# Optimization experiments

Hardware: AMD Instinct MI355X
Metric: run time of the kernel (lower is better)

The kernel has to match this reference:

```python
import jax, jax.numpy as jnp
import numpy as np

B, L, C = 128, 512, 321
PRED = 336
S = 4
K = 25  # moving_avg kernel
EPS = 1e-5
N = L // S          # 128
H = 2048 // S       # 512


def setup_inputs() -> dict:
    key = jax.random.key(0)
    ks = jax.random.split(key, 16)
    def w(k, shape, fan_in):
        return jax.random.uniform(k, shape, jnp.float32, -1.0, 1.0) / np.sqrt(fan_in)
    return {
        "x": jax.random.normal(ks[0], (B, L, C), jnp.float32),
        "revin_w": jnp.ones((C,), jnp.float32),
        "revin_b": jnp.zeros((C,), jnp.float32),
        "W11": w(ks[1], (N, H), N), "b11": w(ks[2], (H,), N),
        "W12": w(ks[3], (H, N), H), "b12": w(ks[4], (N,), H),
        "W21": w(ks[5], (N, H), N), "b21": w(ks[6], (H,), N),
        "W22": w(ks[7], (H, N), H), "b22": w(ks[8], (N,), H),
        "W_tr": w(ks[9], (L, PRED), L), "b_tr": w(ks[10], (PRED,), L),
        "W_se": w(ks[11], (L, PRED), L), "b_se": w(ks[12], (PRED,), L),
    }


def reference(x, revin_w, revin_b, W11, b11, W12, b12, W21, b21, W22, b22,
              W_tr, b_tr, W_se, b_se):
    # RevIN norm (statistics are detached in the original)
    mean = jax.lax.stop_gradient(jnp.mean(x, axis=1, keepdims=True))
    std = jax.lax.stop_gradient(
        jnp.sqrt(jnp.var(x, axis=1, keepdims=True) + EPS))
    xn = (x - mean) / std * revin_w + revin_b  # [B, L, C]

    # Decomp: replicate-pad along time then moving average of width K
    front = jnp.repeat(xn[:, 0:1, :], K - 1 - (K - 1) // 2, axis=1)
    end = jnp.repeat(xn[:, -1:, :], (K - 1) // 2, axis=1)
    padded = jnp.concatenate([front, xn, end], axis=1)  # [B, L+K-1, C]
    cs = jnp.concatenate(
        [jnp.zeros((B, 1, C), padded.dtype), jnp.cumsum(padded, axis=1)], axis=1)
    trend = (cs[:, K:, :] - cs[:, :-K, :]) / K  # [B, L, C]
    seasonal = xn - trend

    trend_p = jnp.transpose(trend, (0, 2, 1))      # [B, C, L]
    seasonal_p = jnp.transpose(seasonal, (0, 2, 1))  # [B, C, L]

    # Trend head: Linear L -> PRED
    trend_out = jnp.einsum('bcl,lp->bcp', trend_p, W_tr) + b_tr

    # Seasonal head: Splitting (strided interleave) = reshape + transpose
    xs = seasonal_p.reshape(B, C, N, S).transpose(0, 1, 3, 2)  # [B, C, S, N]
    h = jnp.matmul(jax.nn.gelu(jnp.matmul(xs, W11) + b11, approximate=False), W12) + b12
    h = jnp.matmul(jax.nn.gelu(jnp.matmul(h, W21) + b21, approximate=False), W22) + b22
    # Catting is the exact inverse interleave
    sea = h.transpose(0, 1, 3, 2).reshape(B, C, L)  # [B, C, L]
    sea_out = jnp.einsum('bcl,lp->bcp', sea, W_se) + b_se

    out = jnp.transpose(trend_out + sea_out, (0, 2, 1))  # [B, PRED, C]

    # RevIN denorm
    out = (out - revin_b) / (revin_w + EPS * EPS)
    out = out * std + mean
    return out
```

## Files before the change

### kernel.cpp

```cpp
#include <hip/hip_runtime.h>
#include <math.h>

#define BB   128
#define LL   512
#define CC   321
#define PREDD 336

using bf16x8  = __attribute__((ext_vector_type(8))) __bf16;
using floatx4 = __attribute__((ext_vector_type(4))) float;
using uintx4  = __attribute__((ext_vector_type(4))) unsigned int;
typedef unsigned short u16;
typedef unsigned int u32;

#define MFMA16(a,b,c) __builtin_amdgcn_mfma_f32_16x16x32_bf16(a,b,c,0,0,0)

__device__ __forceinline__ u16 f2bf(float f){
    union { float f; unsigned u; } v; v.f = f;
    unsigned r = v.u + 0x7FFFu + ((v.u >> 16) & 1u);
    return (u16)(r >> 16);
}

__device__ __forceinline__ float fgelu(float x){
    float u = x*(0.7978845608f + 0.035677408f*x*x);
    float a = fminf(u*2.8853900818f, 80.f);
    float t = __builtin_amdgcn_exp2f(a);
    return x*t*__builtin_amdgcn_rcpf(1.f + t);
}

__device__ __forceinline__ int swz128(int r, int s){ return r*128 + (((s & 8) | ((s ^ r) & 7)) << 3); }
__device__ __forceinline__ int swz64 (int r, int s){ return r*64  + (((s ^ r) & 7) << 3); }

__device__ __forceinline__ void dma16(const u16* g, const u16* l){
    __builtin_amdgcn_global_load_lds(
        (const __attribute__((address_space(1))) u32*)g,
        (__attribute__((address_space(3))) u32*)l, 16, 0, 0);
}

__global__ void prep_k(const float* __restrict__ W11, const float* __restrict__ W12,
                       const float* __restrict__ W21, const float* __restrict__ W22,
                       const float* __restrict__ Wtr, const float* __restrict__ Wse,
                       u16* __restrict__ BT1, u16* __restrict__ BT2,
                       u16* __restrict__ BT3, u16* __restrict__ BT4,
                       u16* __restrict__ BT5)
{
    int idx = blockIdx.x * 256 + threadIdx.x;
    if (idx < 65536){
        int h = idx >> 7, k = idx & 127;
        BT1[idx] = f2bf(W11[k*512 + h]);
        BT3[idx] = f2bf(W21[k*512 + h]);
        int n = idx >> 9, k2 = idx & 511;
        BT2[idx] = f2bf(W12[k2*128 + n]);
        BT4[idx] = f2bf(W22[k2*128 + n]);
    }
    if (idx < 393216){
        int p = idx >> 10, k = idx & 1023;
        float v = 0.f;
        if (p < PREDD){
            if (k < 512) v = Wtr[k*PREDD + p];
            else { int kk = k - 512; int s = kk >> 7; int n = kk & 127; v = Wse[(4*n + s)*PREDD + p]; }
        }
        BT5[idx] = f2bf(v);
    }
}

#define XT(t,c) xt[((t)<<4) + (((t)>>5)<<1) + (c)]
__global__ __launch_bounds__(256) void decomp_k(
    const float* __restrict__ x, const float* __restrict__ rw, const float* __restrict__ rb,
    u16* __restrict__ Afin, u16* __restrict__ xs, float2* __restrict__ stats)
{
    __shared__ float xt[8240];
    __shared__ float red[2][16][16];
    __shared__ float sh_m[16], sh_istd[16];
    int b = blockIdx.x / 21, ct = blockIdx.x % 21;
    int tid = threadIdx.x;

    int cl = tid & 15, lp = tid >> 4;
    int c = ct*16 + cl;
    bool valid = c < CC;
    const float* xb = x + (size_t)b*LL*CC;
    float s = 0.f, q = 0.f;
    for (int i = 0; i < 32; ++i){
        int t = lp + 16*i;
        float v = valid ? xb[(size_t)t*CC + c] : 0.f;
        XT(t, cl) = v;
        s += v; q += v*v;
    }
    red[0][lp][cl] = s; red[1][lp][cl] = q;
    __syncthreads();
    if (tid < 16){
        float ss = 0.f, qq = 0.f;
        for (int j = 0; j < 16; ++j){ ss += red[0][j][tid]; qq += red[1][j][tid]; }
        float m  = ss * (1.f/512.f);
        float var = qq * (1.f/512.f) - m*m;
        float sd = sqrtf(var + 1e-5f);
        sh_m[tid] = m; sh_istd[tid] = 1.f/sd;
        int cc = ct*16 + tid;
        if (cc < CC) stats[(size_t)b*CC + cc] = make_float2(m, sd);
    }
    __syncthreads();

    int ch = tid >> 4, tp = tid & 15;
    int c2 = ct*16 + ch;
    if (c2 >= CC) return;
    float m = sh_m[ch], istd = sh_istd[ch];
    float w = rw[c2] * istd, bbv = rb[c2];
    size_t bc = (size_t)b*CC + c2;
    u16* tr  = Afin + bc*1024;
    u16* xsr = xs   + bc*512;
    int t0 = tp*32;

    float win = 0.f;
#pragma unroll
    for (int d = -12; d <= 12; ++d){
        int u = t0 + d; u = u < 0 ? 0 : (u > 511 ? 511 : u);
        win += XT(u, ch);
    }
    u16 trbuf[8];
    u16 xsbuf[4][8];
#pragma unroll
    for (int i = 0; i < 32; ++i){
        int t = t0 + i;
        float Ax = win * (1.f/25.f);
        float xv = XT(t, ch);
        trbuf[i & 7] = f2bf((Ax - m)*w + bbv);
        xsbuf[i & 3][i >> 2] = f2bf((xv - Ax)*w);
        if ((i & 7) == 7)
            *(uintx4*)(tr + t0 + (i & ~7)) = *(const uintx4*)trbuf;
        int uo = t - 12; uo = uo < 0 ? 0 : uo;
        int un = t + 13; un = un > 511 ? 511 : un;
        win += XT(un, ch) - XT(uo, ch);
    }
#pragma unroll
    for (int s4 = 0; s4 < 4; ++s4)
        *(uintx4*)(xsr + s4*128 + tp*8) = *(const uintx4*)xsbuf[s4];
}

#define RW1 0
#define RH  8192
#define RW2 16384
__global__ __launch_bounds__(256, 2) void mlp_fused_k(
    const u16* __restrict__ xs,
    const u16* __restrict__ BT1, const float* __restrict__ b11,
    const u16* __restrict__ BT2, const float* __restrict__ b12,
    const u16* __restrict__ BT3, const float* __restrict__ b21,
    const u16* __restrict__ BT4, const float* __restrict__ b22,
    u16* __restrict__ Afin)
{
    __shared__ u16 lds[32768];
    const int tid = threadIdx.x;
    const int row0 = blockIdx.x * 128;
    const int lane = tid & 63;
    const int wv = tid >> 6;
    const int wm = wv & 1, wn = wv >> 1;
    const int quad = lane >> 4, cl = lane & 15;

#pragma unroll
    for (int i = 0; i < 8; ++i){
        int qq = (wv*8 + i)*64 + lane;
        int r = qq >> 4, sp = qq & 15;
        int s = (sp & 8) | ((sp ^ r) & 7);
        dma16(xs + (size_t)(row0 + r)*128 + s*8, lds + RW2 + qq*8);
    }
    __syncthreads();

    bf16x8 afrag[4][4];
#pragma unroll
    for (int mt = 0; mt < 4; ++mt)
#pragma unroll
        for (int ks = 0; ks < 4; ++ks)
            afrag[mt][ks] = *(const bf16x8*)(lds + RW2 + swz128(wm*64 + mt*16 + cl, ks*4 + quad));
    __syncthreads();

#pragma unroll
    for (int i = 0; i < 4; ++i){
        int qq = (wv*4 + i)*64 + lane;
        { int r = qq >> 4, sp = qq & 15; int s = (sp & 8) | ((sp ^ r) & 7);
          dma16(BT1 + (size_t)r*128 + s*8, lds + RW1 + qq*8); }
        { int r = qq >> 3, p = qq & 7; int s = (p ^ r) & 7;
          dma16(BT2 + (size_t)r*512 + s*8, lds + RW2 + qq*8); }
    }
    __syncthreads();

    for (int mlp = 0; mlp < 2; ++mlp){
        const float* ba = mlp ? b21 : b11;
        const float* bb = mlp ? b22 : b12;

        floatx4 Yacc[16];
#pragma unroll
        for (int i = 0; i < 16; ++i) Yacc[i] = (floatx4){0.f,0.f,0.f,0.f};

        for (int hc = 0; hc < 8; ++hc){
            const int g = mlp*8 + hc;
            floatx4 hacc[8];
#pragma unroll
            for (int i = 0; i < 8; ++i) hacc[i] = (floatx4){0.f,0.f,0.f,0.f};
#pragma unroll
            for (int ks = 0; ks < 4; ++ks){
                bf16x8 b0 = *(const bf16x8*)(lds + RW1 + swz128(wn*32 + cl,      ks*4 + quad));
                bf16x8 b1 = *(const bf16x8*)(lds + RW1 + swz128(wn*32 + 16 + cl, ks*4 + quad));
#pragma unroll
                for (int mt = 0; mt < 4; ++mt){
                    hacc[mt*2+0] = MFMA16(afrag[mt][ks], b0, hacc[mt*2+0]);
                    hacc[mt*2+1] = MFMA16(afrag[mt][ks], b1, hacc[mt*2+1]);
                }
            }
            {
                int h0 = wn*32 + cl, h1v = h0 + 16;
                float bav0 = ba[hc*64 + h0];
                float bav1 = ba[hc*64 + h1v];
#pragma unroll
                for (int mt = 0; mt < 4; ++mt){
                    floatx4 v0 = hacc[mt*2], v1 = hacc[mt*2+1];
#pragma unroll
                    for (int i = 0; i < 4; ++i){
                        int r = wm*64 + mt*16 + quad*4 + i;
                        lds[RH + r*64 + (((h0 >> 3) ^ r) & 7)*8 + (h0 & 7)]   = f2bf(fgelu(v0[i] + bav0));
                        lds[RH + r*64 + (((h1v >> 3) ^ r) & 7)*8 + (h1v & 7)] = f2bf(fgelu(v1[i] + bav1));
                    }
                }
            }
            __syncthreads();
            if (g < 15){
                const u16* w1s = ((g+1) & 8) ? BT3 : BT1;
                const u16* w2s = ((g+1) & 8) ? BT4 : BT2;
                const int hb = ((g+1) & 7) * 64;
                const int slot = RW2 + ((hc+1) & 1) * 8192;
#pragma unroll
                for (int i = 0; i < 4; ++i){
                    int qq = (wv*4 + i)*64 + lane;
                    if (hc < 7){
                        int r = qq >> 4, sp = qq & 15; int s = (sp & 8) | ((sp ^ r) & 7);
                        dma16(w1s + (size_t)(hb + r)*128 + s*8, lds + RW1 + qq*8);
                    }
                    int r2 = qq >> 3, p2 = qq & 7; int s2 = (p2 ^ r2) & 7;
                    dma16(w2s + (size_t)r2*512 + hb + s2*8, lds + slot + qq*8);
                }
            }
            {
                const int W2p = RW2 + (hc & 1) * 8192;
#pragma unroll
                for (int ks = 0; ks < 2; ++ks){
                    bf16x8 a2[4], b2[4];
#pragma unroll
                    for (int mt = 0; mt < 4; ++mt) a2[mt] = *(const bf16x8*)(lds + RH  + swz64(wm*64 + mt*16 + cl, ks*4 + quad));
#pragma unroll
                    for (int nt = 0; nt < 4; ++nt) b2[nt] = *(const bf16x8*)(lds + W2p + swz64(wn*64 + nt*16 + cl, ks*4 + quad));
#pragma unroll
                    for (int mt = 0; mt < 4; ++mt)
#pragma unroll
                        for (int nt = 0; nt < 4; ++nt)
                            Yacc[mt*4+nt] = MFMA16(a2[mt], b2[nt], Yacc[mt*4+nt]);
                }
            }
            __syncthreads();
        }

        if (mlp == 0){
#pragma unroll
            for (int mt = 0; mt < 4; ++mt)
#pragma unroll
                for (int nt = 0; nt < 4; ++nt){
                    int c = wn*64 + nt*16 + cl;
                    float bv = bb[c];
                    floatx4 v = Yacc[mt*4+nt];
#pragma unroll
                    for (int i = 0; i < 4; ++i){
                        int r = wm*64 + mt*16 + quad*4 + i;
                        lds[swz128(r, c >> 3) + (c & 7)] = f2bf(v[i] + bv);
                    }
                }
            __syncthreads();
#pragma unroll
            for (int mt = 0; mt < 4; ++mt)
#pragma unroll
                for (int ks = 0; ks < 4; ++ks)
                    afrag[mt][ks] = *(const bf16x8*)(lds + swz128(wm*64 + mt*16 + cl, ks*4 + quad));
            __syncthreads();
#pragma unroll
            for (int i = 0; i < 4; ++i){
                int qq = (wv*4 + i)*64 + lane;
                int r = qq >> 4, sp = qq & 15; int s = (sp & 8) | ((sp ^ r) & 7);
                dma16(BT3 + (size_t)r*128 + s*8, lds + RW1 + qq*8);
            }
            __syncthreads();
        } else {
#pragma unroll
            for (int mt = 0; mt < 4; ++mt)
#pragma unroll
                for (int nt = 0; nt < 4; ++nt){
                    int c = wn*64 + nt*16 + cl;
                    float bv = bb[c];
                    floatx4 v = Yacc[mt*4+nt];
#pragma unroll
                    for (int i = 0; i < 4; ++i){
                        int gr = row0 + wm*64 + mt*16 + quad*4 + i;
                        Afin[(size_t)(gr>>2)*1024 + 512 + (size_t)(gr&3)*128 + c] = f2bf(v[i] + bv);
                    }
                }
        }
    }
}

__global__ __launch_bounds__(256, 2) void head_gemm_k(
    const u16* __restrict__ A, const u16* __restrict__ BT,
    float* __restrict__ Cf,
    const float* __restrict__ bias, const float* __restrict__ bias2,
    const float* __restrict__ rw, const float* __restrict__ rb,
    const float2* __restrict__ stats)
{
    __shared__ u16 lds[32768];
    const int id = blockIdx.x;
    const int xcd = id & 7, slot = id >> 3;
    const int g8 = slot / 3, j = slot - g8*3;
    const int by = xcd + 8*g8;
    if (by >= 321) return;
    const int row0 = by * 128, col0 = j * 128;

    const int tid = threadIdx.x;
    const int lane = tid & 63;
    const int wv = tid >> 6;
    const int wm = wv & 1, wn = wv >> 1;
    const int quad = lane >> 4, cl = lane & 15;

    const int qbase = wv*4*64 + lane;

#pragma unroll
    for (int i = 0; i < 4; ++i){
        int qq = qbase + i*64;
        int r = qq >> 3, p = qq & 7; int s = (p ^ r) & 7;
        dma16(A  + (size_t)(row0 + r)*1024 + s*8, lds + qq*8);
        dma16(BT + (size_t)(col0 + r)*1024 + s*8, lds + 16384 + qq*8);
    }
    __syncthreads();

    floatx4 acc[16];
#pragma unroll
    for (int i = 0; i < 16; ++i) acc[i] = (floatx4){0.f,0.f,0.f,0.f};

    for (int it = 0; it < 16; ++it){
        const int cur = (it & 1) * 8192;
        if (it < 15){
            const int nxt = ((it+1) & 1) * 8192;
            const int k0 = (it+1) * 64;
#pragma unroll
            for (int i = 0; i < 4; ++i){
                int qq = qbase + i*64;
                int r = qq >> 3, p = qq & 7; int s = (p ^ r) & 7;
                dma16(A  + (size_t)(row0 + r)*1024 + k0 + s*8, lds + nxt + qq*8);
                dma16(BT + (size_t)(col0 + r)*1024 + k0 + s*8, lds + 16384 + nxt + qq*8);
            }
        }
#pragma unroll
        for (int kk = 0; kk < 2; ++kk){
            bf16x8 af[4], bfr[4];
#pragma unroll
            for (int mt = 0; mt < 4; ++mt) af[mt]  = *(const bf16x8*)(lds + cur + swz64(wm*64 + mt*16 + cl, kk*4 + quad));
#pragma unroll
            for (int nt = 0; nt < 4; ++nt) bfr[nt] = *(const bf16x8*)(lds + 16384 + cur + swz64(wn*64 + nt*16 + cl, kk*4 + quad));
#pragma unroll
            for (int mt = 0; mt < 4; ++mt)
#pragma unroll
                for (int nt = 0; nt < 4; ++nt)
                    acc[mt*4+nt] = MFMA16(af[mt], bfr[nt], acc[mt*4+nt]);
        }
        __syncthreads();
    }

#pragma unroll
    for (int mt = 0; mt < 4; ++mt)
#pragma unroll
        for (int nt = 0; nt < 4; ++nt){
            floatx4 v = acc[mt*4+nt];
            int gc = col0 + wn*64 + nt*16 + cl;
            if (gc >= PREDD) continue;
            float bsum = bias[gc] + bias2[gc];
#pragma unroll
            for (int i = 0; i < 4; ++i){
                int gr = row0 + wm*64 + mt*16 + quad*4 + i;
                float val = v[i] + bsum;
                int bv2 = gr / CC;
                int c  = gr - bv2*CC;
                val = (val - rb[c]) / (rw[c] + 1e-10f);
                float2 st = stats[gr];
                val = val*st.y + st.x;
                Cf[(size_t)bv2*(PREDD*CC) + (size_t)gc*CC + c] = val;
            }
        }
}

extern "C" void kernel_launch(void* const* d_in, const int* in_sizes, int n_in,
                              void* d_out, int out_size, void* d_ws, size_t ws_size,
                              hipStream_t stream)
{
    const float* x   = (const float*)d_in[0];
    const float* rvw = (const float*)d_in[1];
    const float* rvb = (const float*)d_in[2];
    const float* W11 = (const float*)d_in[3];
    const float* b11 = (const float*)d_in[4];
    const float* W12 = (const float*)d_in[5];
    const float* b12 = (const float*)d_in[6];
    const float* W21 = (const float*)d_in[7];
    const float* b21 = (const float*)d_in[8];
    const float* W22 = (const float*)d_in[9];
    const float* b22 = (const float*)d_in[10];
    const float* Wtr = (const float*)d_in[11];
    const float* btr = (const float*)d_in[12];
    const float* Wse = (const float*)d_in[13];
    const float* bse = (const float*)d_in[14];
    float* out = (float*)d_out;

    char* ws = (char*)d_ws;
    u16* BT1 = (u16*)(ws + 0);
    u16* BT2 = (u16*)(ws + 131072);
    u16* BT3 = (u16*)(ws + 262144);
    u16* BT4 = (u16*)(ws + 393216);
    u16* BT5 = (u16*)(ws + 524288);
    float2* stats = (float2*)(ws + 1310720);
    u16* Afin = (u16*)(ws + 1639424);
    u16* xs   = (u16*)(ws + 85787648);

    hipLaunchKernelGGL(prep_k, dim3(1536), dim3(256), 0, stream,
                       W11, W12, W21, W22, Wtr, Wse, BT1, BT2, BT3, BT4, BT5);
    hipLaunchKernelGGL(decomp_k, dim3(128*21), dim3(256), 0, stream,
                       x, rvw, rvb, Afin, xs, stats);
    hipLaunchKernelGGL(mlp_fused_k, dim3(1284), dim3(256), 0, stream,
                       xs, BT1, b11, BT2, b12, BT3, b21, BT4, b22, Afin);
    hipLaunchKernelGGL(head_gemm_k, dim3(984), dim3(256), 0, stream,
                       Afin, BT5, out, btr, bse, rvw, rvb, stats);
}
```

Before: 514.0 us.

## Give each wave private hidden scratch and double-buffer weight chunks in fused MLP

Result: faster. 451.2 us (-12.2%).

```diff
diff --git a/kernel.cpp b/kernel.cpp
--- a/kernel.cpp
+++ b/kernel.cpp
@@ -135,9 +135,8 @@
         *(uintx4*)(xsr + s4*128 + tp*8) = *(const uintx4*)xsbuf[s4];
 }
 
-#define RW1 0
-#define RH  8192
-#define RW2 16384
+#define SL1 16384
+#define HS  32768
 __global__ __launch_bounds__(256, 2) void mlp_fused_k(
     const u16* __restrict__ xs,
     const u16* __restrict__ BT1, const float* __restrict__ b11,
@@ -146,159 +145,142 @@
     const u16* __restrict__ BT4, const float* __restrict__ b22,
     u16* __restrict__ Afin)
 {
-    __shared__ u16 lds[32768];
+    __shared__ u16 lds[40960];
     const int tid = threadIdx.x;
     const int row0 = blockIdx.x * 128;
     const int lane = tid & 63;
     const int wv = tid >> 6;
-    const int wm = wv & 1, wn = wv >> 1;
     const int quad = lane >> 4, cl = lane & 15;
-
-#pragma unroll
-    for (int i = 0; i < 8; ++i){
-        int qq = (wv*8 + i)*64 + lane;
-        int r = qq >> 4, sp = qq & 15;
-        int s = (sp & 8) | ((sp ^ r) & 7);
-        dma16(xs + (size_t)(row0 + r)*128 + s*8, lds + RW2 + qq*8);
-    }
-    __syncthreads();
-
-    bf16x8 afrag[4][4];
-#pragma unroll
-    for (int mt = 0; mt < 4; ++mt)
-#pragma unroll
-        for (int ks = 0; ks < 4; ++ks)
-            afrag[mt][ks] = *(const bf16x8*)(lds + RW2 + swz128(wm*64 + mt*16 + cl, ks*4 + quad));
-    __syncthreads();
+    const int wrow = row0 + wv*32;
+    u16* hscr = lds + HS + wv*2048;
+    const int rdswz = ((cl >> 2) & 3) << 4;
 
 #pragma unroll
     for (int i = 0; i < 4; ++i){
         int qq = (wv*4 + i)*64 + lane;
         { int r = qq >> 4, sp = qq & 15; int s = (sp & 8) | ((sp ^ r) & 7);
-          dma16(BT1 + (size_t)r*128 + s*8, lds + RW1 + qq*8); }
+          dma16(BT1 + (size_t)r*128 + s*8, lds + qq*8); }
         { int r = qq >> 3, p = qq & 7; int s = (p ^ r) & 7;
-          dma16(BT2 + (size_t)r*512 + s*8, lds + RW2 + qq*8); }
-    }
+          dma16(BT2 + (size_t)r*512 + s*8, lds + 8192 + qq*8); }
+    }
+    bf16x8 afrag[2][4];
+#pragma unroll
+    for (int mt = 0; mt < 2; ++mt)
+#pragma unroll
+        for (int ks = 0; ks < 4; ++ks)
+            afrag[mt][ks] = *(const bf16x8*)(xs + (size_t)(wrow + mt*16 + cl)*128 + ks*32 + quad*8);
+
+    floatx4 Yacc[16];
+#pragma unroll
+    for (int i = 0; i < 16; ++i) Yacc[i] = (floatx4){0.f,0.f,0.f,0.f};
+
     __syncthreads();
 
-    for (int mlp = 0; mlp < 2; ++mlp){
-        const float* ba = mlp ? b21 : b11;
-        const float* bb = mlp ? b22 : b12;
-
-        floatx4 Yacc[16];
-#pragma unroll
-        for (int i = 0; i < 16; ++i) Yacc[i] = (floatx4){0.f,0.f,0.f,0.f};
-
-        for (int hc = 0; hc < 8; ++hc){
-            const int g = mlp*8 + hc;
-            floatx4 hacc[8];
-#pragma unroll
-            for (int i = 0; i < 8; ++i) hacc[i] = (floatx4){0.f,0.f,0.f,0.f};
-#pragma unroll
-            for (int ks = 0; ks < 4; ++ks){
-                bf16x8 b0 = *(const bf16x8*)(lds + RW1 + swz128(wn*32 + cl,      ks*4 + quad));
-                bf16x8 b1 = *(const bf16x8*)(lds + RW1 + swz128(wn*32 + 16 + cl, ks*4 + quad));
-#pragma unroll
-                for (int mt = 0; mt < 4; ++mt){
-                    hacc[mt*2+0] = MFMA16(afrag[mt][ks], b0, hacc[mt*2+0]);
-                    hacc[mt*2+1] = MFMA16(afrag[mt][ks], b1, hacc[mt*2+1]);
-                }
-            }
-            {
-                int h0 = wn*32 + cl, h1v = h0 + 16;
-                float bav0 = ba[hc*64 + h0];
-                float bav1 = ba[hc*64 + h1v];
-#pragma unroll
-                for (int mt = 0; mt < 4; ++mt){
-                    floatx4 v0 = hacc[mt*2], v1 = hacc[mt*2+1];
-#pragma unroll
-                    for (int i = 0; i < 4; ++i){
-                        int r = wm*64 + mt*16 + quad*4 + i;
-                        lds[RH + r*64 + (((h0 >> 3) ^ r) & 7)*8 + (h0 & 7)]   = f2bf(fgelu(v0[i] + bav0));
-                        lds[RH + r*64 + (((h1v >> 3) ^ r) & 7)*8 + (h1v & 7)] = f2bf(fgelu(v1[i] + bav1));
-                    }
-                }
-            }
-            __syncthreads();
-            if (g < 15){
-                const u16* w1s = ((g+1) & 8) ? BT3 : BT1;
-                const u16* w2s = ((g+1) & 8) ? BT4 : BT2;
-                const int hb = ((g+1) & 7) * 64;
-                const int slot = RW2 + ((hc+1) & 1) * 8192;
-#pragma unroll
-                for (int i = 0; i < 4; ++i){
-                    int qq = (wv*4 + i)*64 + lane;
-                    if (hc < 7){
-                        int r = qq >> 4, sp = qq & 15; int s = (sp & 8) | ((sp ^ r) & 7);
-                        dma16(w1s + (size_t)(hb + r)*128 + s*8, lds + RW1 + qq*8);
-                    }
-                    int r2 = qq >> 3, p2 = qq & 7; int s2 = (p2 ^ r2) & 7;
-                    dma16(w2s + (size_t)r2*512 + hb + s2*8, lds + slot + qq*8);
-                }
-            }
-            {
-                const int W2p = RW2 + (hc & 1) * 8192;
-#pragma unroll
-                for (int ks = 0; ks < 2; ++ks){
-                    bf16x8 a2[4], b2[4];
-#pragma unroll
-                    for (int mt = 0; mt < 4; ++mt) a2[mt] = *(const bf16x8*)(lds + RH  + swz64(wm*64 + mt*16 + cl, ks*4 + quad));
-#pragma unroll
-                    for (int nt = 0; nt < 4; ++nt) b2[nt] = *(const bf16x8*)(lds + W2p + swz64(wn*64 + nt*16 + cl, ks*4 + quad));
-#pragma unroll
-                    for (int mt = 0; mt < 4; ++mt)
-#pragma unroll
-                        for (int nt = 0; nt < 4; ++nt)
-                            Yacc[mt*4+nt] = MFMA16(a2[mt], b2[nt], Yacc[mt*4+nt]);
-                }
-            }
-            __syncthreads();
-        }
-
-        if (mlp == 0){
-#pragma unroll
-            for (int mt = 0; mt < 4; ++mt)
-#pragma unroll
-                for (int nt = 0; nt < 4; ++nt){
-                    int c = wn*64 + nt*16 + cl;
-                    float bv = bb[c];
-                    floatx4 v = Yacc[mt*4+nt];
-#pragma unroll
-                    for (int i = 0; i < 4; ++i){
-                        int r = wm*64 + mt*16 + quad*4 + i;
-                        lds[swz128(r, c >> 3) + (c & 7)] = f2bf(v[i] + bv);
-                    }
-                }
-            __syncthreads();
-#pragma unroll
-            for (int mt = 0; mt < 4; ++mt)
-#pragma unroll
-                for (int ks = 0; ks < 4; ++ks)
-                    afrag[mt][ks] = *(const bf16x8*)(lds + swz128(wm*64 + mt*16 + cl, ks*4 + quad));
-            __syncthreads();
+    for (int g = 0; g < 16; ++g){
+        const int cur = (g & 1) ? SL1 : 0;
+        const int nxt = (g & 1) ? 0 : SL1;
+        if (g < 15){
+            const u16* w1s = ((g+1) & 8) ? BT3 : BT1;
+            const u16* w2s = ((g+1) & 8) ? BT4 : BT2;
+            const int hb = ((g+1) & 7) * 64;
 #pragma unroll
             for (int i = 0; i < 4; ++i){
                 int qq = (wv*4 + i)*64 + lane;
-                int r = qq >> 4, sp = qq & 15; int s = (sp & 8) | ((sp ^ r) & 7);
-                dma16(BT3 + (size_t)r*128 + s*8, lds + RW1 + qq*8);
-            }
-            __syncthreads();
-        } else {
-#pragma unroll
-            for (int mt = 0; mt < 4; ++mt)
-#pragma unroll
-                for (int nt = 0; nt < 4; ++nt){
-                    int c = wn*64 + nt*16 + cl;
-                    float bv = bb[c];
-                    floatx4 v = Yacc[mt*4+nt];
-#pragma unroll
-                    for (int i = 0; i < 4; ++i){
-                        int gr = row0 + wm*64 + mt*16 + quad*4 + i;
-                        Afin[(size_t)(gr>>2)*1024 + 512 + (size_t)(gr&3)*128 + c] = f2bf(v[i] + bv);
+                { int r = qq >> 4, sp = qq & 15; int s = (sp & 8) | ((sp ^ r) & 7);
+                  dma16(w1s + (size_t)(hb + r)*128 + s*8, lds + nxt + qq*8); }
+                { int r = qq >> 3, p = qq & 7; int s = (p ^ r) & 7;
+                  dma16(w2s + (size_t)r*512 + hb + s*8, lds + nxt + 8192 + qq*8); }
+            }
+        }
+        const float* ba = (g & 8) ? b21 : b11;
+        const int hc = g & 7;
+
+        floatx4 hacc[8];
+#pragma unroll
+        for (int i = 0; i < 8; ++i) hacc[i] = (floatx4){0.f,0.f,0.f,0.f};
+#pragma unroll
+        for (int ks = 0; ks < 4; ++ks){
+            bf16x8 bfr[4];
+#pragma unroll
+            for (int nt = 0; nt < 4; ++nt)
+                bfr[nt] = *(const bf16x8*)(lds + cur + swz128(nt*16 + cl, ks*4 + quad));
+#pragma unroll
+            for (int mt = 0; mt < 2; ++mt)
+#pragma unroll
+                for (int nt = 0; nt < 4; ++nt)
+                    hacc[mt*4+nt] = MFMA16(afrag[mt][ks], bfr[nt], hacc[mt*4+nt]);
+        }
+#pragma unroll
+        for (int mt = 0; mt < 2; ++mt)
+#pragma unroll
+            for (int nt = 0; nt < 4; ++nt){
+                floatx4 v = hacc[mt*4+nt];
+                int h = nt*16 + cl;
+                float bav = ba[hc*64 + h];
+#pragma unroll
+                for (int i = 0; i < 4; ++i){
+                    int r = mt*16 + quad*4 + i;
+                    hscr[r*64 + (h ^ (quad << 4))] = f2bf(fgelu(v[i] + bav));
+                }
+            }
+#pragma unroll
+        for (int ks = 0; ks < 2; ++ks){
+            bf16x8 a2[2];
+#pragma unroll
+            for (int mt = 0; mt < 2; ++mt)
+                a2[mt] = *(const bf16x8*)(hscr + (mt*16 + cl)*64 + ((ks*32 + quad*8) ^ rdswz));
+#pragma unroll
+            for (int nt = 0; nt < 8; ++nt){
+                bf16x8 b2 = *(const bf16x8*)(lds + cur + 8192 + swz64(nt*16 + cl, ks*4 + quad));
+#pragma unroll
+                for (int mt = 0; mt < 2; ++mt)
+                    Yacc[mt*8+nt] = MFMA16(a2[mt], b2, Yacc[mt*8+nt]);
+            }
+        }
+        __syncthreads();
+
+        if (g == 7){
+#pragma unroll
+            for (int half = 0; half < 2; ++half){
+#pragma unroll
+                for (int mt = 0; mt < 2; ++mt)
+#pragma unroll
+                    for (int nt = 0; nt < 4; ++nt){
+                        int ntg = half*4 + nt;
+                        floatx4 v = Yacc[mt*8+ntg];
+                        int c = ntg*16 + cl;
+                        float bv = b12[c];
+                        int h = nt*16 + cl;
+#pragma unroll
+                        for (int i = 0; i < 4; ++i){
+                            int r = mt*16 + quad*4 + i;
+                            hscr[r*64 + (h ^ (quad << 4))] = f2bf(v[i] + bv);
+                        }
                     }
-                }
-        }
-    }
+#pragma unroll
+                for (int mt = 0; mt < 2; ++mt)
+#pragma unroll
+                    for (int k2 = 0; k2 < 2; ++k2)
+                        afrag[mt][half*2 + k2] = *(const bf16x8*)(hscr + (mt*16 + cl)*64 + ((k2*32 + quad*8) ^ rdswz));
+            }
+#pragma unroll
+            for (int i = 0; i < 16; ++i) Yacc[i] = (floatx4){0.f,0.f,0.f,0.f};
+        }
+    }
+
+#pragma unroll
+    for (int mt = 0; mt < 2; ++mt)
+#pragma unroll
+        for (int nt = 0; nt < 8; ++nt){
+            int c = nt*16 + cl;
+            float bv = b22[c];
+            floatx4 v = Yacc[mt*8+nt];
+#pragma unroll
+            for (int i = 0; i < 4; ++i){
+                int gr = wrow + mt*16 + quad*4 + i;
+                Afin[(size_t)(gr>>2)*1024 + 512 + (size_t)(gr&3)*128 + c] = f2bf(v[i] + bv);
+            }
+        }
 }
 
 __global__ __launch_bounds__(256, 2) void head_gemm_k(
```
